# Optimization experiments

Hardware: AMD Instinct MI355X
Metric: run time of the kernel (lower is better)

## Reference

```python
import jax, jax.numpy as jnp
import numpy as np

B, T, D = 8, 4096, 768

def setup_inputs() -> dict:
    key = jax.random.key(0)
    k1, k2, k3, k4, k5, k6 = jax.random.split(key, 6)
    inputs = jax.random.normal(k1, (B, T, D), dtype=jnp.float32)
    mask = jax.random.randint(k2, (B, T), 0, 2, dtype=jnp.int32)
    s = 1.0 / np.sqrt(D)
    Wq_w = jax.random.normal(k3, (D, D), dtype=jnp.float32) * s
    Wq_b = jax.random.normal(k4, (D,), dtype=jnp.float32) * 0.02
    Wk_w = jax.random.normal(k5, (D, D), dtype=jnp.float32) * s
    Wk_b = jax.random.normal(k6, (D,), dtype=jnp.float32) * 0.02
    return {"inputs": inputs, "mask": mask, "Wq_w": Wq_w, "Wq_b": Wq_b, "Wk_w": Wk_w, "Wk_b": Wk_b}

def reference(inputs, mask, Wq_w, Wq_b, Wk_w, Wk_b):
    # Linear layers (torch: x @ W.T + b)
    query = jnp.einsum('btd,ed->bte', inputs, Wq_w) + Wq_b  # (b,t,d)
    key = jnp.einsum('btd,ed->bte', inputs, Wk_w) + Wk_b    # (b,t,d)
    d_k = query.shape[-1]
    scores = jnp.einsum('bqd,bkd->bqk', query, key) / jnp.sqrt(jnp.float32(d_k))  # (b,t,t)
    # mask.unsqueeze(1): (b,1,t) broadcast over query rows
    scores = jnp.where(mask[:, None, :] == 0, jnp.float32(-1e9), scores)
    weights = jax.nn.softmax(scores, axis=2)  # (b,t,t)
    # einsum 'btd,btt->bd' == diagonal of weights, weighted sum of inputs
    w_diag = jnp.einsum('btt->bt', weights)   # (b,t)
    outputs = jnp.einsum('btd,bt->bd', inputs, w_diag)  # (b,d)
    return outputs
```

## Files before the change

kernel.cpp:

```cpp
#include <hip/hip_runtime.h>

#define BB 8
#define TT 4096
#define DD 768
#define MM (BB*TT)

typedef _Float16 f16;
typedef _Float16 f16x8 __attribute__((ext_vector_type(8)));
typedef float f32x4 __attribute__((ext_vector_type(4)));

typedef __attribute__((address_space(1))) void void_g;
typedef __attribute__((address_space(3))) void void_l;

__device__ __forceinline__ void gload16(const void* g, void* l) {
  __builtin_amdgcn_global_load_lds((void_g*)g, (void_l*)l, 16, 0, 0);
}

__global__ void cvt2_f32_f16(const float* __restrict__ a, const float* __restrict__ b,
                             f16* __restrict__ oa, f16* __restrict__ ob, int n) {
  int i = (blockIdx.x * blockDim.x + threadIdx.x) * 8;
  if (i >= 2 * n) return;
  const float* src = (i < n) ? a : b;
  f16* dst = (i < n) ? oa : ob;
  const int j = (i < n) ? i : i - n;
  float4 x = *(const float4*)(src + j);
  float4 y = *(const float4*)(src + j + 4);
  f16x8 o;
  o[0] = (f16)x.x; o[1] = (f16)x.y; o[2] = (f16)x.z; o[3] = (f16)x.w;
  o[4] = (f16)y.x; o[5] = (f16)y.y; o[6] = (f16)y.z; o[7] = (f16)y.w;
  *(f16x8*)(dst + j) = o;
}

__global__ __launch_bounds__(256)
void compact_mask(const int* __restrict__ mask, int* __restrict__ idx,
                  int* __restrict__ nbv) {
  __shared__ int wcnt[4];
  const int b = blockIdx.x;
  const int w = threadIdx.x >> 6, l = threadIdx.x & 63;
  const int* mb = mask + b * TT + w * 1024;
  int mv[16];
  unsigned long long bal[16];
#pragma unroll
  for (int c = 0; c < 16; ++c) {
    mv[c] = mb[c * 64 + l];
    bal[c] = __ballot(mv[c] != 0);
  }
  int tot = 0;
#pragma unroll
  for (int c = 0; c < 16; ++c) tot += __popcll(bal[c]);
  if (l == 0) wcnt[w] = tot;
  __syncthreads();
  int base = 0;
  for (int ww = 0; ww < w; ++ww) base += wcnt[ww];
#pragma unroll
  for (int c = 0; c < 16; ++c) {
    const int pre = __popcll(bal[c] & ((1ull << l) - 1ull));
    if (mv[c]) idx[b * TT + base + pre] = w * 1024 + c * 64 + l;
    base += __popcll(bal[c]);
  }
  if (w == 3 && l == 0) nbv[b] = base;
}

__global__ __launch_bounds__(256)
void gather_cvt(const float* __restrict__ X, const int* __restrict__ idx,
                const int* __restrict__ nbv, f16* __restrict__ Xc) {
  const int rr = blockIdx.x * 8 + (threadIdx.x >> 5);
  const int b = rr >> 12, j = rr & 4095;
  const int l = threadIdx.x & 31;
  if (j >= nbv[b]) return;
  const float* src = X + ((size_t)b * TT + idx[b * TT + j]) * DD + l * 24;
  f16* dst = Xc + ((size_t)b * TT + j) * DD + l * 24;
#pragma unroll
  for (int c = 0; c < 3; ++c) {
    float4 a = *(const float4*)(src + c * 8);
    float4 d4 = *(const float4*)(src + c * 8 + 4);
    f16x8 o;
    o[0] = (f16)a.x;  o[1] = (f16)a.y;  o[2] = (f16)a.z;  o[3] = (f16)a.w;
    o[4] = (f16)d4.x; o[5] = (f16)d4.y; o[6] = (f16)d4.z; o[7] = (f16)d4.w;
    *(f16x8*)(dst + c * 8) = o;
  }
}

__global__ __launch_bounds__(256, 2)
void proj_qkc2(const f16* __restrict__ Xc,
               const f16* __restrict__ Wqh, const f16* __restrict__ Wkh,
               const float* __restrict__ bq, const float* __restrict__ bk,
               const int* __restrict__ nbv,
               f16* __restrict__ Qf, f16* __restrict__ Kc) {
  const int b  = blockIdx.x >> 6;
  const int m0 = (blockIdx.x & 63) * 64;
  const int nb = nbv[b];
  if (m0 >= ((nb + 63) & ~63)) return;

  __shared__ f16 As[4][64 * 32];
  __shared__ f16 Ws[4][256 * 32];
  const int isK = blockIdx.z;
  const f16* Wh = isK ? Wkh : Wqh;
  const float* bias = isK ? bk : bq;
  const int n0 = blockIdx.y * 256;
  const int t = threadIdx.x;
  const int lane = t & 63;
  const int w = t >> 6;
  const int wn = w * 64;
  const int fr = lane & 15, fq = lane >> 4;
  const int xrd = ((fr >> 1) & 3) << 3;

  f32x4 acc[4][4] = {};

  const int r0 = t >> 2;
  const int c8 = ((t & 3) ^ ((t >> 3) & 3)) * 8;
  const f16* w0 = Wh + (size_t)(n0 + r0) * DD + c8;
  const f16* a0 = Xc + (size_t)b * TT * DD + (size_t)(m0 + r0) * DD + c8;

#define PSTAGE(sl, ks_) do { \
    const int k0_ = (ks_) * 32; \
    gload16(a0 + k0_,                      &As[sl][w * 512]); \
    gload16(w0 + k0_,                      &Ws[sl][w * 512]); \
    gload16(w0 + (size_t)64  * DD + k0_,   &Ws[sl][2048 + w * 512]); \
    gload16(w0 + (size_t)128 * DD + k0_,   &Ws[sl][4096 + w * 512]); \
    gload16(w0 + (size_t)192 * DD + k0_,   &Ws[sl][6144 + w * 512]); \
  } while (0)

  PSTAGE(0, 0);
  PSTAGE(1, 1);
  asm volatile("s_waitcnt vmcnt(5)" ::: "memory");
  __builtin_amdgcn_sched_barrier(0);
  __builtin_amdgcn_s_barrier();

  for (int ks = 0; ks < 24; ++ks) {
    const int sl = ks & 3;
    if (ks + 2 < 24) {
      PSTAGE((ks + 2) & 3, ks + 2);
      asm volatile("s_waitcnt vmcnt(10)" ::: "memory");
    } else if (ks + 1 < 24) {
      asm volatile("s_waitcnt vmcnt(5)" ::: "memory");
    } else {
      asm volatile("s_waitcnt vmcnt(0)" ::: "memory");
    }
    __builtin_amdgcn_sched_barrier(0);
    __builtin_amdgcn_s_barrier();
    __builtin_amdgcn_sched_barrier(0);

    f16x8 a[4], bfr[4];
#pragma unroll
    for (int i = 0; i < 4; ++i)
      a[i] = *(const f16x8*)&As[sl][(((i * 16 + fr) * 32) + fq * 8) ^ xrd];
#pragma unroll
    for (int j = 0; j < 4; ++j)
      bfr[j] = *(const f16x8*)&Ws[sl][(((wn + j * 16 + fr) * 32) + fq * 8) ^ xrd];
    __builtin_amdgcn_s_setprio(1);
#pragma unroll
    for (int i = 0; i < 4; ++i)
#pragma unroll
      for (int j = 0; j < 4; ++j)
        acc[i][j] = __builtin_amdgcn_mfma_f32_16x16x32_f16(a[i], bfr[j], acc[i][j], 0, 0, 0);
    __builtin_amdgcn_s_setprio(0);
    __builtin_amdgcn_sched_barrier(0);
    __builtin_amdgcn_s_barrier();
  }
#undef PSTAGE

#pragma unroll
  for (int j = 0; j < 4; ++j) {
    const int col = n0 + wn + j * 16 + fr;
    const float bv = bias[col];
#pragma unroll
    for (int i = 0; i < 4; ++i) {
#pragma unroll
      for (int r = 0; r < 4; ++r) {
        const int rowc = m0 + i * 16 + fq * 4 + r;
        const f16 v = (f16)(acc[i][j][r] + bv);
        if (!isK) {
          const size_t q = (size_t)b * TT * DD +
              ((((size_t)(rowc >> 6) * 24 + (col >> 5)) * 4 + ((rowc >> 4) & 3)) * 512 +
               ((rowc & 15) + (((col >> 3) & 3) << 4)) * 8 + (col & 7));
          Qf[q] = v;
        } else {
          Kc[(size_t)b * TT * DD + (size_t)rowc * DD + col] = v;
        }
      }
    }
  }
}

__global__ __launch_bounds__(256, 3)
void attn17(const f16* __restrict__ Qf, const f16* __restrict__ K,
            const int* __restrict__ nbv, float* __restrict__ pzv,
            float* __restrict__ sdg) {
  const int bid = blockIdx.x;
  const int qs = bid / 48;
  const int rem = bid % 48;
  const int kh = rem >> 3;
  const int bb = rem & 7;
  const int nb = nbv[bb];
  if (qs * 128 >= nb) return;

  __shared__ f16 Ks[2][128 * 64];
  const int t = threadIdx.x, l = t & 63, w = t >> 6;
  const int wq = w >> 1, wk = w & 1;
  const int fr = l & 15, fq = l >> 4;
  const int q0 = qs * 128;
  const float scale = 0.036084391824351613f;
  const int nkt = (nb + 127) >> 7;
  const int q6 = nkt / 6, r6 = nkt % 6;
  const int cnt = q6 + (kh < r6 ? 1 : 0);
  const int lo  = kh * q6 + (kh < r6 ? kh : r6);
  const int P = cnt * 12;

  const f16* Kg = K + (size_t)bb * TT * DD;
  const f16* qf = Qf + (size_t)bb * TT * DD + (size_t)(qs * 2 + wq) * 49152 + (size_t)l * 8;

  const int c8 = ((t & 3) ^ ((t >> 3) & 3)) * 8;
  const f16* klo = Kg + (size_t)(t >> 2) * DD + c8;
  const f16* khi = klo + (size_t)64 * DD;

  const int sx = (fq ^ ((fr >> 1) & 3)) * 8;
  const int bbase = (wk * 64 + fr) * 32 + sx;

  f32x4 acc[4][4] = {};
  f32x4 zacc[4] = {};
  int im0 = 0, im1 = 0, im2 = 0, im3 = 0;
  f16x8 avA[4], avB[4];

#define STAGE(bf, p_) do { \
    const size_t o0 = (size_t)(lo + (p_) / 12) * 128 * DD + (size_t)(((p_) % 12) * 64); \
    gload16(klo + o0,      &Ks[bf][w * 512]); \
    gload16(khi + o0,      &Ks[bf][2048 + w * 512]); \
    gload16(klo + o0 + 32, &Ks[bf][4096 + w * 512]); \
    gload16(khi + o0 + 32, &Ks[bf][6144 + w * 512]); \
  } while (0)

#define QLOAD(dst, dc_) do { \
    const f16* qp_ = qf + (size_t)(dc_) * 2048; \
    _Pragma("unroll") \
    for (int i = 0; i < 4; ++i) (dst)[i] = *(const f16x8*)(qp_ + i * 512); \
  } while (0)

#define MFMA_ALL(av_, bufv, off_) do { \
    f16x8 bv[4]; \
    _Pragma("unroll") \
    for (int j = 0; j < 4; ++j) bv[j] = *(const f16x8*)&Ks[bufv][(off_) + bbase + j * 512]; \
    __builtin_amdgcn_s_setprio(1); \
    _Pragma("unroll") \
    for (int i = 0; i < 4; ++i) \
      _Pragma("unroll") \
      for (int j = 0; j < 4; ++j) \
        acc[i][j] = __builtin_amdgcn_mfma_f32_16x16x32_f16((av_)[i], bv[j], acc[i][j], 0, 0, 0); \
    __builtin_amdgcn_s_setprio(0); \
  } while (0)

#define KT_EPILOGUE(kt_) do { \
    const float mb0 = im0 ? 0.f : -1e30f; \
    const float mb1 = im1 ? 0.f : -1e30f; \
    const float mb2 = im2 ? 0.f : -1e30f; \
    const float mb3 = im3 ? 0.f : -1e30f; \
    const bool isdiag = ((kt_) == qs); \
    _Pragma("unroll") \
    for (int i = 0; i < 4; ++i) { \
      _Pragma("unroll") \
      for (int rg = 0; rg < 4; ++rg) { \
        float v0 = fmaf(acc[i][0][rg], scale, mb0); \
        float v1 = fmaf(acc[i][1][rg], scale, mb1); \
        float v2 = fmaf(acc[i][2][rg], scale, mb2); \
        float v3 = fmaf(acc[i][3][rg], scale, mb3); \
        if (isdiag) { \
          const int rl = wq * 64 + i * 16 + fq * 4 + rg; \
          const int cl = wk * 64 + fr; \
          if (cl      == rl) sdg[(size_t)bb * TT + q0 + rl] = v0; \
          if (cl + 16 == rl) sdg[(size_t)bb * TT + q0 + rl] = v1; \
          if (cl + 32 == rl) sdg[(size_t)bb * TT + q0 + rl] = v2; \
          if (cl + 48 == rl) sdg[(size_t)bb * TT + q0 + rl] = v3; \
        } \
        zacc[i][rg] += __expf(v0) + __expf(v1) + __expf(v2) + __expf(v3); \
      } \
    } \
    _Pragma("unroll") \
    for (int i = 0; i < 4; ++i) \
      _Pragma("unroll") \
      for (int j = 0; j < 4; ++j) acc[i][j] = (f32x4)(0.f); \
  } while (0)

  STAGE(0, 0);
  QLOAD(avA, 0);
  __syncthreads();

  for (int p = 0; p < P; ++p) {
    const int buf = p & 1;
    const int kt = lo + p / 12, c = p % 12;
    if (c == 0) {
      const int cb0 = kt * 128 + wk * 64 + fr;
      im0 = (cb0 < nb); im1 = (cb0 + 16 < nb);
      im2 = (cb0 + 32 < nb); im3 = (cb0 + 48 < nb);
    }

    QLOAD(avB, 2 * c + 1);
    if (p + 1 < P) STAGE(buf ^ 1, p + 1);
    MFMA_ALL(avA, buf, 0);

    if (p + 1 < P) QLOAD(avA, 2 * (((p + 1) % 12)));
    MFMA_ALL(avB, buf, 4096);

    if (c == 11) KT_EPILOGUE(kt);

    __syncthreads();
  }
#undef STAGE
#undef QLOAD
#undef MFMA_ALL
#undef KT_EPILOGUE

  const int slot = kh * 2 + wk;
#pragma unroll
  for (int i = 0; i < 4; ++i) {
#pragma unroll
    for (int rg = 0; rg < 4; ++rg) {
      float z = zacc[i][rg];
#pragma unroll
      for (int off = 1; off < 16; off <<= 1) z += __shfl_xor(z, off);
      if (fr == 0) {
        const int row = wq * 64 + i * 16 + fq * 4 + rg;
        pzv[(size_t)slot * MM + bb * TT + q0 + row] = z;
      }
    }
  }
}

__global__ void merge12c(const float* __restrict__ pz, const float* __restrict__ sdg,
                         const int* __restrict__ nbv,
                         float* __restrict__ wdiagc, float* __restrict__ out) {
  int i = blockIdx.x * 256 + threadIdx.x;
  if (i < BB * DD) out[i] = 0.f;
  if (i >= MM) return;
  const int b = i >> 12, j = i & 4095;
  if (j >= nbv[b]) { wdiagc[i] = 0.f; return; }
  float Z = 0.f;
#pragma unroll
  for (int s = 0; s < 12; ++s) Z += pz[(size_t)s * MM + i];
  wdiagc[i] = __expf(sdg[i]) / Z;
}

__global__ __launch_bounds__(256)
void out_gemv_c(const f16* __restrict__ Xc, const float* __restrict__ wdiagc,
                const int* __restrict__ nbv, float* __restrict__ out) {
  __shared__ float wsm[256];
  const int b = blockIdx.z;
  const int nb = nbv[b];
  const int tbase = blockIdx.x * 256;
  if (tbase >= nb) return;
  const int d = blockIdx.y * 256 + threadIdx.x;
  wsm[threadIdx.x] = (tbase + threadIdx.x < nb) ? wdiagc[b * TT + tbase + threadIdx.x] : 0.f;
  __syncthreads();
  float acc = 0.f;
  const f16* xp = Xc + (size_t)(b * TT + tbase) * DD + d;
  const int lim = (nb - tbase < 256) ? (nb - tbase) : 256;
  for (int i = 0; i < lim; ++i) acc += (float)xp[(size_t)i * DD] * wsm[i];
  atomicAdd(&out[b * DD + d], acc);
}

__global__ __launch_bounds__(256, 3)
void proj_qk(const float* __restrict__ Af,
             const f16* __restrict__ Wqh, const f16* __restrict__ Wkh,
             const float* __restrict__ bq, const float* __restrict__ bk,
             f16* __restrict__ Qf, f16* __restrict__ Kh) {
  __shared__ f16 As[2][64 * 32];
  __shared__ f16 Ws[2][256 * 32];
  const int isK = blockIdx.z;
  const f16* Wh = isK ? Wkh : Wqh;
  const float* bias = isK ? bk : bq;
  const int m0 = blockIdx.x * 64;
  const int n0 = blockIdx.y * 256;
  const int t = threadIdx.x;
  const int lane = t & 63;
  const int w = t >> 6;
  const int wn = w * 64;
  const int fr = lane & 15, fq = lane >> 4;
  const int xst = ((t >> 3) & 3) << 3;
  const int xrd = ((fr >> 1) & 3) << 3;
  f32x4 acc[4][4] = {};
  const int r0 = t >> 2, cA = (t & 3) * 8;
  const int e0 = t * 8;
  const int c8 = ((t & 3) ^ ((t >> 3) & 3)) * 8;
  const f16* w0 = Wh + (size_t)(n0 + r0) * DD + c8;

#define PSTAGE(bf, ks_) do { \
    const int k0_ = (ks_) * 32; \
    gload16(w0 + k0_,                      &Ws[bf][w * 512]); \
    gload16(w0 + (size_t)64  * DD + k0_,   &Ws[bf][2048 + w * 512]); \
    gload16(w0 + (size_t)128 * DD + k0_,   &Ws[bf][4096 + w * 512]); \
    gload16(w0 + (size_t)192 * DD + k0_,   &Ws[bf][6144 + w * 512]); \
    { \
      const float* g0 = Af + (size_t)(m0 + r0) * DD + k0_ + cA; \
      float4 x0 = *(const float4*)g0, x1 = *(const float4*)(g0 + 4); \
      f16x8 va; \
      va[0] = (f16)x0.x; va[1] = (f16)x0.y; va[2] = (f16)x0.z; va[3] = (f16)x0.w; \
      va[4] = (f16)x1.x; va[5] = (f16)x1.y; va[6] = (f16)x1.z; va[7] = (f16)x1.w; \
      *(f16x8*)&As[bf][e0 ^ xst] = va; \
    } \
  } while (0)

  PSTAGE(0, 0);
  __syncthreads();
  for (int ks = 0; ks < 24; ++ks) {
    const int bf = ks & 1;
    if (ks + 1 < 24) PSTAGE(bf ^ 1, ks + 1);
    f16x8 a[4], b[4];
#pragma unroll
    for (int i = 0; i < 4; ++i)
      a[i] = *(const f16x8*)&As[bf][(((i * 16 + fr) * 32) + fq * 8) ^ xrd];
#pragma unroll
    for (int j = 0; j < 4; ++j)
      b[j] = *(const f16x8*)&Ws[bf][(((wn + j * 16 + fr) * 32) + fq * 8) ^ xrd];
#pragma unroll
    for (int i = 0; i < 4; ++i)
#pragma unroll
      for (int j = 0; j < 4; ++j)
        acc[i][j] = __builtin_amdgcn_mfma_f32_16x16x32_f16(a[i], b[j], acc[i][j], 0, 0, 0);
    __syncthreads();
  }
#undef PSTAGE
#pragma unroll
  for (int j = 0; j < 4; ++j) {
    const int col = n0 + wn + j * 16 + fr;
    const float bv = bias[col];
#pragma unroll
    for (int i = 0; i < 4; ++i) {
#pragma unroll
      for (int r = 0; r < 4; ++r) {
        const int row = m0 + i * 16 + fq * 4 + r;
        const f16 v = (f16)(acc[i][j][r] + bv);
        if (!isK) {
          const size_t idxq = (((size_t)(row >> 6) * 24 + (col >> 5)) * 4 +
                              ((row >> 4) & 3)) * 512 +
                             ((row & 15) + (((col >> 3) & 3) << 4)) * 8 + (col & 7);
          Qf[idxq] = v;
        } else {
          Kh[(size_t)row * DD + col] = v;
        }
      }
    }
  }
}

__global__ __launch_bounds__(256, 3)
void attn15(const f16* __restrict__ Qf, const f16* __restrict__ K,
            const int* __restrict__ mask, float* __restrict__ pzv,
            float* __restrict__ sdg) {
  __shared__ f16 Ks[2][128 * 64];
  const int bid = blockIdx.x;
  const int qs = bid / 24;
  const int kh = (bid % 24) >> 3;
  const int bb = bid & 7;
  const int t = threadIdx.x, l = t & 63, w = t >> 6;
  const int wq = w >> 1, wk = w & 1;
  const int fr = l & 15, fq = l >> 4;
  const int q0 = qs * 128;
  const float scale = 0.036084391824351613f;
  const int lo = kh * 11;
  const int cnt = (kh < 2) ? 11 : 10;
  const int P = cnt * 12;
  const f16* Kg = K + (size_t)bb * TT * DD;
  const int grp = bb * 64 + qs * 2 + wq;
  const f16* qf = Qf + (size_t)grp * 24 * 4 * 512 + (size_t)l * 8;
  const int c8 = ((t & 3) ^ ((t >> 3) & 3)) * 8;
  const f16* klo = Kg + (size_t)(t >> 2) * DD + c8;
  const f16* khi = klo + (size_t)64 * DD;
  const int sx = (fq ^ ((fr >> 1) & 3)) * 8;
  const int bbase = (wk * 64 + fr) * 32 + sx;
  f32x4 acc[4][4] = {};
  f32x4 zacc[4] = {};
  int im0 = 1, im1 = 1, im2 = 1, im3 = 1;
  f16x8 avA[4], avB[4];

#define STAGE(bf, p_) do { \
    const size_t o0 = (size_t)(lo + (p_) / 12) * 128 * DD + (size_t)(((p_) % 12) * 64); \
    gload16(klo + o0,      &Ks[bf][w * 512]); \
    gload16(khi + o0,      &Ks[bf][2048 + w * 512]); \
    gload16(klo + o0 + 32, &Ks[bf][4096 + w * 512]); \
    gload16(khi + o0 + 32, &Ks[bf][6144 + w * 512]); \
  } while (0)
#define QLOAD(dst, dc_) do { \
    const f16* qp_ = qf + (size_t)(dc_) * 2048; \
    _Pragma("unroll") \
    for (int i = 0; i < 4; ++i) (dst)[i] = *(const f16x8*)(qp_ + i * 512); \
  } while (0)
#define MFMA_ALL(av_, bufv, off_) do { \
    f16x8 bv[4]; \
    _Pragma("unroll") \
    for (int j = 0; j < 4; ++j) bv[j] = *(const f16x8*)&Ks[bufv][(off_) + bbase + j * 512]; \
    __builtin_amdgcn_s_setprio(1); \
    _Pragma("unroll") \
    for (int i = 0; i < 4; ++i) \
      _Pragma("unroll") \
      for (int j = 0; j < 4; ++j) \
        acc[i][j] = __builtin_amdgcn_mfma_f32_16x16x32_f16((av_)[i], bv[j], acc[i][j], 0, 0, 0); \
    __builtin_amdgcn_s_setprio(0); \
  } while (0)
#define KT_EPILOGUE(kt_) do { \
    const float mb0 = im0 ? 0.f : -1e30f; \
    const float mb1 = im1 ? 0.f : -1e30f; \
    const float mb2 = im2 ? 0.f : -1e30f; \
    const float mb3 = im3 ? 0.f : -1e30f; \
    const bool isdiag = ((kt_) == qs); \
    _Pragma("unroll") \
    for (int i = 0; i < 4; ++i) { \
      _Pragma("unroll") \
      for (int rg = 0; rg < 4; ++rg) { \
        float v0 = fmaf(acc[i][0][rg], scale, mb0); \
        float v1 = fmaf(acc[i][1][rg], scale, mb1); \
        float v2 = fmaf(acc[i][2][rg], scale, mb2); \
        float v3 = fmaf(acc[i][3][rg], scale, mb3); \
        if (isdiag) { \
          const int rl = wq * 64 + i * 16 + fq * 4 + rg; \
          const int cl = wk * 64 + fr; \
          if (cl      == rl) sdg[(size_t)bb * TT + q0 + rl] = v0; \
          if (cl + 16 == rl) sdg[(size_t)bb * TT + q0 + rl] = v1; \
          if (cl + 32 == rl) sdg[(size_t)bb * TT + q0 + rl] = v2; \
          if (cl + 48 == rl) sdg[(size_t)bb * TT + q0 + rl] = v3; \
        } \
        zacc[i][rg] += __expf(v0) + __expf(v1) + __expf(v2) + __expf(v3); \
      } \
    } \
    _Pragma("unroll") \
    for (int i = 0; i < 4; ++i) \
      _Pragma("unroll") \
      for (int j = 0; j < 4; ++j) acc[i][j] = (f32x4)(0.f); \
  } while (0)

  STAGE(0, 0);
  QLOAD(avA, 0);
  __syncthreads();
  for (int p = 0; p < P; ++p) {
    const int buf = p & 1;
    const int kt = lo + p / 12, c = p % 12;
    if (c == 0) {
      const int kb = bb * TT + kt * 128 + wk * 64 + fr;
      im0 = mask[kb]; im1 = mask[kb + 16]; im2 = mask[kb + 32]; im3 = mask[kb + 48];
    }
    QLOAD(avB, 2 * c + 1);
    if (p + 1 < P) STAGE(buf ^ 1, p + 1);
    MFMA_ALL(avA, buf, 0);
    if (p + 1 < P) QLOAD(avA, 2 * (((p + 1) % 12)));
    MFMA_ALL(avB, buf, 4096);
    if (c == 11) KT_EPILOGUE(kt);
    __syncthreads();
  }
#undef STAGE
#undef QLOAD
#undef MFMA_ALL
#undef KT_EPILOGUE
  const int slot = kh * 2 + wk;
#pragma unroll
  for (int i = 0; i < 4; ++i) {
#pragma unroll
    for (int rg = 0; rg < 4; ++rg) {
      float z = zacc[i][rg];
#pragma unroll
      for (int off = 1; off < 16; off <<= 1) z += __shfl_xor(z, off);
      if (fr == 0) {
        const int row = wq * 64 + i * 16 + fq * 4 + rg;
        pzv[(size_t)slot * MM + bb * TT + q0 + row] = z;
      }
    }
  }
}

__global__ void merge6(const float* __restrict__ pz, const float* __restrict__ sdg,
                       float* __restrict__ wdiag, float* __restrict__ out) {
  int i = blockIdx.x * 256 + threadIdx.x;
  if (i < BB * DD) out[i] = 0.f;
  if (i >= MM) return;
  float Z = 0.f;
#pragma unroll
  for (int s = 0; s < 6; ++s) Z += pz[(size_t)s * MM + i];
  wdiag[i] = __expf(sdg[i]) / Z;
}

__global__ __launch_bounds__(256)
void out_gemv(const float* __restrict__ X, const float* __restrict__ wdiag,
              float* __restrict__ out) {
  __shared__ float wsm[256];
  const int b = blockIdx.z;
  const int d = blockIdx.y * 256 + threadIdx.x;
  const int tbase = blockIdx.x * 256;
  wsm[threadIdx.x] = wdiag[b * TT + tbase + threadIdx.x];
  __syncthreads();
  float acc = 0.f;
  const float* xp = X + (size_t)(b * TT + tbase) * DD + d;
#pragma unroll 4
  for (int i = 0; i < 256; ++i) acc += xp[(size_t)i * DD] * wsm[i];
  atomicAdd(&out[b * DD + d], acc);
}

extern "C" void kernel_launch(void* const* d_in, const int* in_sizes, int n_in,
                              void* d_out, int out_size, void* d_ws, size_t ws_size,
                              hipStream_t stream) {
  const float* X    = (const float*)d_in[0];
  const int*   mask = (const int*)d_in[1];
  const float* Wq_w = (const float*)d_in[2];
  const float* Wq_b = (const float*)d_in[3];
  const float* Wk_w = (const float*)d_in[4];
  const float* Wk_b = (const float*)d_in[5];
  float* out = (float*)d_out;

  const size_t n2 = (size_t)MM * DD;
  const size_t wde = (size_t)DD * DD;

  char* p = (char*)d_ws;
  f16* Qf = (f16*)p;            p += n2 * sizeof(f16);
  f16* Kc = (f16*)p;            p += n2 * sizeof(f16);
  f16* Xc = (f16*)p;            p += n2 * sizeof(f16);
  f16* Wqh = (f16*)p;           p += wde * sizeof(f16);
  f16* Wkh = (f16*)p;           p += wde * sizeof(f16);
  int* idx = (int*)p;           p += (size_t)MM * sizeof(int);
  int* nbv = (int*)p;           p += 64;
  float* pz = (float*)p;        p += (size_t)12 * MM * sizeof(float);
  float* sdg = (float*)p;       p += (size_t)MM * sizeof(float);
  float* wdiagc = (float*)p;    p += (size_t)MM * sizeof(float);
  const size_t need_new = (size_t)(p - (char*)d_ws);
  const bool useNew = ws_size >= need_new;

  if (useNew) {
    compact_mask<<<8, 256, 0, stream>>>(mask, idx, nbv);
    cvt2_f32_f16<<<576, 256, 0, stream>>>(Wq_w, Wk_w, Wqh, Wkh, DD * DD);
    gather_cvt<<<4096, 256, 0, stream>>>(X, idx, nbv, Xc);
    proj_qkc2<<<dim3(512, 3, 2), 256, 0, stream>>>(Xc, Wqh, Wkh, Wq_b, Wk_b,
                                                   nbv, Qf, Kc);
    attn17<<<1536, 256, 0, stream>>>(Qf, Kc, nbv, pz, sdg);
    merge12c<<<128, 256, 0, stream>>>(pz, sdg, nbv, wdiagc, out);
    out_gemv_c<<<dim3(16, 3, 8), 256, 0, stream>>>(Xc, wdiagc, nbv, out);
  } else {
    f16* Qf2 = (f16*)d_ws;
    f16* Kh2 = Qf2 + n2;
    f16* Wqh2 = Kh2 + n2;
    f16* Wkh2 = Wqh2 + wde;
    float* pz2 = (float*)Wqh2;
    float* sdg2 = pz2 + 6 * (size_t)MM;
    float* wdiag2 = sdg2 + MM;
    cvt2_f32_f16<<<576, 256, 0, stream>>>(Wq_w, Wk_w, Wqh2, Wkh2, DD * DD);
    proj_qk<<<dim3(512, 3, 2), 256, 0, stream>>>(X, Wqh2, Wkh2, Wq_b, Wk_b,
                                                 Qf2, Kh2);
    attn15<<<768, 256, 0, stream>>>(Qf2, Kh2, mask, pz2, sdg2);
    merge6<<<128, 256, 0, stream>>>(pz2, sdg2, wdiag2, out);
    out_gemv<<<dim3(16, 3, 8), 256, 0, stream>>>(X, wdiag2, out);
  }
}
```

Measured before the change: 258.3 us.

## Fold Wq·Wk into one matrix and use compacted X as keys

Rewrites the scores as X Wq^T Wk X^T plus key-side bias terms. It precomputes M = Wq^T Wk with a small GEMM, projects only Y = X M, and uses the compacted f16 X directly as K. Terms that are constant per query row cancel in the softmax, so only a per-key bias vector (bq·Wk·x) is added in the attention epilogue. This halves the projection GEMM work and removes the K buffer, at the cost of small extra kernels and different f16 rounding of the product matrix. The old fallback path is dropped.

Result: no change. 261.4 us (+1.2%).

```diff
diff --git a/kernel.cpp b/kernel.cpp
--- a/kernel.cpp
+++ b/kernel.cpp
@@ -14,21 +14,6 @@
 
 __device__ __forceinline__ void gload16(const void* g, void* l) {
   __builtin_amdgcn_global_load_lds((void_g*)g, (void_l*)l, 16, 0, 0);
-}
-
-__global__ void cvt2_f32_f16(const float* __restrict__ a, const float* __restrict__ b,
-                             f16* __restrict__ oa, f16* __restrict__ ob, int n) {
-  int i = (blockIdx.x * blockDim.x + threadIdx.x) * 8;
-  if (i >= 2 * n) return;
-  const float* src = (i < n) ? a : b;
-  f16* dst = (i < n) ? oa : ob;
-  const int j = (i < n) ? i : i - n;
-  float4 x = *(const float4*)(src + j);
-  float4 y = *(const float4*)(src + j + 4);
-  f16x8 o;
-  o[0] = (f16)x.x; o[1] = (f16)x.y; o[2] = (f16)x.z; o[3] = (f16)x.w;
-  o[4] = (f16)y.x; o[5] = (f16)y.y; o[6] = (f16)y.z; o[7] = (f16)y.w;
-  *(f16x8*)(dst + j) = o;
 }
 
 __global__ __launch_bounds__(256)
@@ -62,14 +47,44 @@
 }
 
 __global__ __launch_bounds__(256)
-void gather_cvt(const float* __restrict__ X, const int* __restrict__ idx,
-                const int* __restrict__ nbv, f16* __restrict__ Xc) {
+void cvt2T(const float* __restrict__ a, const float* __restrict__ b,
+           f16* __restrict__ oaT, f16* __restrict__ obT) {
+  __shared__ float tile[64][65];
+  const float* src = blockIdx.z ? b : a;
+  f16* dst = blockIdx.z ? obT : oaT;
+  const int n0 = blockIdx.x * 64, d0 = blockIdx.y * 64;
+  const int r = threadIdx.x >> 6, c = threadIdx.x & 63;
+#pragma unroll
+  for (int k = 0; k < 16; ++k)
+    tile[k * 4 + r][c] = src[(size_t)(n0 + k * 4 + r) * DD + d0 + c];
+  __syncthreads();
+#pragma unroll
+  for (int k = 0; k < 16; ++k)
+    dst[(size_t)(d0 + k * 4 + r) * DD + n0 + c] = (f16)tile[c][k * 4 + r];
+}
+
+__global__ __launch_bounds__(256)
+void evec_k(const float* __restrict__ Wk, const float* __restrict__ bq,
+            float* __restrict__ e) {
+  const int d = blockIdx.x * 256 + threadIdx.x;
+  float acc = 0.f;
+  for (int n = 0; n < DD; ++n) acc += bq[n] * Wk[(size_t)n * DD + d];
+  e[d] = acc;
+}
+
+__global__ __launch_bounds__(256)
+void gather_cvt2(const float* __restrict__ X, const int* __restrict__ idx,
+                 const int* __restrict__ nbv, const float* __restrict__ e,
+                 f16* __restrict__ Xc, float* __restrict__ vb) {
   const int rr = blockIdx.x * 8 + (threadIdx.x >> 5);
   const int b = rr >> 12, j = rr & 4095;
   const int l = threadIdx.x & 31;
   if (j >= nbv[b]) return;
+  const float scale = 0.036084391824351613f;
   const float* src = X + ((size_t)b * TT + idx[b * TT + j]) * DD + l * 24;
   f16* dst = Xc + ((size_t)b * TT + j) * DD + l * 24;
+  const float* ep = e + l * 24;
+  float vp = 0.f;
 #pragma unroll
   for (int c = 0; c < 3; ++c) {
     float4 a = *(const float4*)(src + c * 8);
@@ -78,25 +93,22 @@
     o[0] = (f16)a.x;  o[1] = (f16)a.y;  o[2] = (f16)a.z;  o[3] = (f16)a.w;
     o[4] = (f16)d4.x; o[5] = (f16)d4.y; o[6] = (f16)d4.z; o[7] = (f16)d4.w;
     *(f16x8*)(dst + c * 8) = o;
-  }
-}
-
-__global__ __launch_bounds__(256, 2)
-void proj_qkc2(const f16* __restrict__ Xc,
-               const f16* __restrict__ Wqh, const f16* __restrict__ Wkh,
-               const float* __restrict__ bq, const float* __restrict__ bk,
-               const int* __restrict__ nbv,
-               f16* __restrict__ Qf, f16* __restrict__ Kc) {
-  const int b  = blockIdx.x >> 6;
-  const int m0 = (blockIdx.x & 63) * 64;
-  const int nb = nbv[b];
-  if (m0 >= ((nb + 63) & ~63)) return;
-
-  __shared__ f16 As[4][64 * 32];
-  __shared__ f16 Ws[4][256 * 32];
-  const int isK = blockIdx.z;
-  const f16* Wh = isK ? Wkh : Wqh;
-  const float* bias = isK ? bk : bq;
+    vp += a.x * ep[c * 8]     + a.y * ep[c * 8 + 1] +
+          a.z * ep[c * 8 + 2] + a.w * ep[c * 8 + 3] +
+          d4.x * ep[c * 8 + 4] + d4.y * ep[c * 8 + 5] +
+          d4.z * ep[c * 8 + 6] + d4.w * ep[c * 8 + 7];
+  }
+#pragma unroll
+  for (int off = 1; off < 32; off <<= 1) vp += __shfl_xor(vp, off);
+  if (l == 0) vb[b * TT + j] = vp * scale;
+}
+
+__global__ __launch_bounds__(256, 3)
+void gemm_mt(const f16* __restrict__ WkT, const f16* __restrict__ WqT,
+             f16* __restrict__ MT) {
+  __shared__ f16 As[2][64 * 32];
+  __shared__ f16 Ws[2][256 * 32];
+  const int m0 = blockIdx.x * 64;
   const int n0 = blockIdx.y * 256;
   const int t = threadIdx.x;
   const int lane = t & 63;
@@ -109,7 +121,75 @@
 
   const int r0 = t >> 2;
   const int c8 = ((t & 3) ^ ((t >> 3) & 3)) * 8;
-  const f16* w0 = Wh + (size_t)(n0 + r0) * DD + c8;
+  const f16* w0 = WqT + (size_t)(n0 + r0) * DD + c8;
+  const f16* a0 = WkT + (size_t)(m0 + r0) * DD + c8;
+
+#define PSTAGE(bf, ks_) do { \
+    const int k0_ = (ks_) * 32; \
+    gload16(a0 + k0_,                      &As[bf][w * 512]); \
+    gload16(w0 + k0_,                      &Ws[bf][w * 512]); \
+    gload16(w0 + (size_t)64  * DD + k0_,   &Ws[bf][2048 + w * 512]); \
+    gload16(w0 + (size_t)128 * DD + k0_,   &Ws[bf][4096 + w * 512]); \
+    gload16(w0 + (size_t)192 * DD + k0_,   &Ws[bf][6144 + w * 512]); \
+  } while (0)
+
+  PSTAGE(0, 0);
+  __syncthreads();
+  for (int ks = 0; ks < 24; ++ks) {
+    const int bf = ks & 1;
+    if (ks + 1 < 24) PSTAGE(bf ^ 1, ks + 1);
+    f16x8 a[4], bfr[4];
+#pragma unroll
+    for (int i = 0; i < 4; ++i)
+      a[i] = *(const f16x8*)&As[bf][(((i * 16 + fr) * 32) + fq * 8) ^ xrd];
+#pragma unroll
+    for (int j = 0; j < 4; ++j)
+      bfr[j] = *(const f16x8*)&Ws[bf][(((wn + j * 16 + fr) * 32) + fq * 8) ^ xrd];
+#pragma unroll
+    for (int i = 0; i < 4; ++i)
+#pragma unroll
+      for (int j = 0; j < 4; ++j)
+        acc[i][j] = __builtin_amdgcn_mfma_f32_16x16x32_f16(a[i], bfr[j], acc[i][j], 0, 0, 0);
+    __syncthreads();
+  }
+#undef PSTAGE
+
+#pragma unroll
+  for (int j = 0; j < 4; ++j) {
+    const int col = n0 + wn + j * 16 + fr;
+#pragma unroll
+    for (int i = 0; i < 4; ++i)
+#pragma unroll
+      for (int r = 0; r < 4; ++r) {
+        const int row = m0 + i * 16 + fq * 4 + r;
+        MT[(size_t)row * DD + col] = (f16)acc[i][j][r];
+      }
+  }
+}
+
+__global__ __launch_bounds__(256, 2)
+void projY(const f16* __restrict__ Xc, const f16* __restrict__ MT,
+           const int* __restrict__ nbv, f16* __restrict__ Yf) {
+  const int b  = blockIdx.x >> 6;
+  const int m0 = (blockIdx.x & 63) * 64;
+  const int nb = nbv[b];
+  if (m0 >= ((nb + 63) & ~63)) return;
+
+  __shared__ f16 As[4][64 * 32];
+  __shared__ f16 Ws[4][256 * 32];
+  const int n0 = blockIdx.y * 256;
+  const int t = threadIdx.x;
+  const int lane = t & 63;
+  const int w = t >> 6;
+  const int wn = w * 64;
+  const int fr = lane & 15, fq = lane >> 4;
+  const int xrd = ((fr >> 1) & 3) << 3;
+
+  f32x4 acc[4][4] = {};
+
+  const int r0 = t >> 2;
+  const int c8 = ((t & 3) ^ ((t >> 3) & 3)) * 8;
+  const f16* w0 = MT + (size_t)(n0 + r0) * DD + c8;
   const f16* a0 = Xc + (size_t)b * TT * DD + (size_t)(m0 + r0) * DD + c8;
 
 #define PSTAGE(sl, ks_) do { \
@@ -163,30 +243,24 @@
 #pragma unroll
   for (int j = 0; j < 4; ++j) {
     const int col = n0 + wn + j * 16 + fr;
-    const float bv = bias[col];
 #pragma unroll
     for (int i = 0; i < 4; ++i) {
 #pragma unroll
       for (int r = 0; r < 4; ++r) {
         const int rowc = m0 + i * 16 + fq * 4 + r;
-        const f16 v = (f16)(acc[i][j][r] + bv);
-        if (!isK) {
-          const size_t q = (size_t)b * TT * DD +
-              ((((size_t)(rowc >> 6) * 24 + (col >> 5)) * 4 + ((rowc >> 4) & 3)) * 512 +
-               ((rowc & 15) + (((col >> 3) & 3) << 4)) * 8 + (col & 7));
-          Qf[q] = v;
-        } else {
-          Kc[(size_t)b * TT * DD + (size_t)rowc * DD + col] = v;
-        }
+        const size_t q = (size_t)b * TT * DD +
+            ((((size_t)(rowc >> 6) * 24 + (col >> 5)) * 4 + ((rowc >> 4) & 3)) * 512 +
+             ((rowc & 15) + (((col >> 3) & 3) << 4)) * 8 + (col & 7));
+        Yf[q] = (f16)acc[i][j][r];
       }
     }
   }
 }
 
 __global__ __launch_bounds__(256, 3)
-void attn17(const f16* __restrict__ Qf, const f16* __restrict__ K,
-            const int* __restrict__ nbv, float* __restrict__ pzv,
-            float* __restrict__ sdg) {
+void attn17b(const f16* __restrict__ Qf, const f16* __restrict__ K,
+             const float* __restrict__ vbias, const int* __restrict__ nbv,
+             float* __restrict__ pzv, float* __restrict__ sdg) {
   const int bid = blockIdx.x;
   const int qs = bid / 48;
   const int rem = bid % 48;
@@ -209,6 +283,7 @@
 
   const f16* Kg = K + (size_t)bb * TT * DD;
   const f16* qf = Qf + (size_t)bb * TT * DD + (size_t)(qs * 2 + wq) * 49152 + (size_t)l * 8;
+  const float* vbp = vbias + bb * TT;
 
   const int c8 = ((t & 3) ^ ((t >> 3) & 3)) * 8;
   const f16* klo = Kg + (size_t)(t >> 2) * DD + c8;
@@ -220,6 +295,7 @@
   f32x4 acc[4][4] = {};
   f32x4 zacc[4] = {};
   int im0 = 0, im1 = 0, im2 = 0, im3 = 0;
+  float vb0 = 0.f, vb1 = 0.f, vb2 = 0.f, vb3 = 0.f;
   f16x8 avA[4], avB[4];
 
 #define STAGE(bf, p_) do { \
@@ -250,10 +326,10 @@
   } while (0)
 
 #define KT_EPILOGUE(kt_) do { \
-    const float mb0 = im0 ? 0.f : -1e30f; \
-    const float mb1 = im1 ? 0.f : -1e30f; \
-    const float mb2 = im2 ? 0.f : -1e30f; \
-    const float mb3 = im3 ? 0.f : -1e30f; \
+    const float mb0 = im0 ? vb0 : -1e30f; \
+    const float mb1 = im1 ? vb1 : -1e30f; \
+    const float mb2 = im2 ? vb2 : -1e30f; \
+    const float mb3 = im3 ? vb3 : -1e30f; \
     const bool isdiag = ((kt_) == qs); \
     _Pragma("unroll") \
     for (int i = 0; i < 4; ++i) { \
@@ -291,6 +367,8 @@
       const int cb0 = kt * 128 + wk * 64 + fr;
       im0 = (cb0 < nb); im1 = (cb0 + 16 < nb);
       im2 = (cb0 + 32 < nb); im3 = (cb0 + 48 < nb);
+      vb0 = vbp[cb0]; vb1 = vbp[cb0 + 16];
+      vb2 = vbp[cb0 + 32]; vb3 = vbp[cb0 + 48];
     }
 
     QLOAD(avB, 2 * c + 1);
@@ -357,240 +435,6 @@
   atomicAdd(&out[b * DD + d], acc);
 }
 
-__global__ __launch_bounds__(256, 3)
-void proj_qk(const float* __restrict__ Af,
-             const f16* __restrict__ Wqh, const f16* __restrict__ Wkh,
-             const float* __restrict__ bq, const float* __restrict__ bk,
-             f16* __restrict__ Qf, f16* __restrict__ Kh) {
-  __shared__ f16 As[2][64 * 32];
-  __shared__ f16 Ws[2][256 * 32];
-  const int isK = blockIdx.z;
-  const f16* Wh = isK ? Wkh : Wqh;
-  const float* bias = isK ? bk : bq;
-  const int m0 = blockIdx.x * 64;
-  const int n0 = blockIdx.y * 256;
-  const int t = threadIdx.x;
-  const int lane = t & 63;
-  const int w = t >> 6;
-  const int wn = w * 64;
-  const int fr = lane & 15, fq = lane >> 4;
-  const int xst = ((t >> 3) & 3) << 3;
-  const int xrd = ((fr >> 1) & 3) << 3;
-  f32x4 acc[4][4] = {};
-  const int r0 = t >> 2, cA = (t & 3) * 8;
-  const int e0 = t * 8;
-  const int c8 = ((t & 3) ^ ((t >> 3) & 3)) * 8;
-  const f16* w0 = Wh + (size_t)(n0 + r0) * DD + c8;
-
-#define PSTAGE(bf, ks_) do { \
-    const int k0_ = (ks_) * 32; \
-    gload16(w0 + k0_,                      &Ws[bf][w * 512]); \
-    gload16(w0 + (size_t)64  * DD + k0_,   &Ws[bf][2048 + w * 512]); \
-    gload16(w0 + (size_t)128 * DD + k0_,   &Ws[bf][4096 + w * 512]); \
-    gload16(w0 + (size_t)192 * DD + k0_,   &Ws[bf][6144 + w * 512]); \
-    { \
-      const float* g0 = Af + (size_t)(m0 + r0) * DD + k0_ + cA; \
-      float4 x0 = *(const float4*)g0, x1 = *(const float4*)(g0 + 4); \
-      f16x8 va; \
-      va[0] = (f16)x0.x; va[1] = (f16)x0.y; va[2] = (f16)x0.z; va[3] = (f16)x0.w; \
-      va[4] = (f16)x1.x; va[5] = (f16)x1.y; va[6] = (f16)x1.z; va[7] = (f16)x1.w; \
-      *(f16x8*)&As[bf][e0 ^ xst] = va; \
-    } \
-  } while (0)
-
-  PSTAGE(0, 0);
-  __syncthreads();
-  for (int ks = 0; ks < 24; ++ks) {
-    const int bf = ks & 1;
-    if (ks + 1 < 24) PSTAGE(bf ^ 1, ks + 1);
-    f16x8 a[4], b[4];
-#pragma unroll
-    for (int i = 0; i < 4; ++i)
-      a[i] = *(const f16x8*)&As[bf][(((i * 16 + fr) * 32) + fq * 8) ^ xrd];
-#pragma unroll
-    for (int j = 0; j < 4; ++j)
-      b[j] = *(const f16x8*)&Ws[bf][(((wn + j * 16 + fr) * 32) + fq * 8) ^ xrd];
-#pragma unroll
-    for (int i = 0; i < 4; ++i)
-#pragma unroll
-      for (int j = 0; j < 4; ++j)
-        acc[i][j] = __builtin_amdgcn_mfma_f32_16x16x32_f16(a[i], b[j], acc[i][j], 0, 0, 0);
-    __syncthreads();
-  }
-#undef PSTAGE
-#pragma unroll
-  for (int j = 0; j < 4; ++j) {
-    const int col = n0 + wn + j * 16 + fr;
-    const float bv = bias[col];
-#pragma unroll
-    for (int i = 0; i < 4; ++i) {
-#pragma unroll
-      for (int r = 0; r < 4; ++r) {
-        const int row = m0 + i * 16 + fq * 4 + r;
-        const f16 v = (f16)(acc[i][j][r] + bv);
-        if (!isK) {
-          const size_t idxq = (((size_t)(row >> 6) * 24 + (col >> 5)) * 4 +
-                              ((row >> 4) & 3)) * 512 +
-                             ((row & 15) + (((col >> 3) & 3) << 4)) * 8 + (col & 7);
-          Qf[idxq] = v;
-        } else {
-          Kh[(size_t)row * DD + col] = v;
-        }
-      }
-    }
-  }
-}
-
-__global__ __launch_bounds__(256, 3)
-void attn15(const f16* __restrict__ Qf, const f16* __restrict__ K,
-            const int* __restrict__ mask, float* __restrict__ pzv,
-            float* __restrict__ sdg) {
-  __shared__ f16 Ks[2][128 * 64];
-  const int bid = blockIdx.x;
-  const int qs = bid / 24;
-  const int kh = (bid % 24) >> 3;
-  const int bb = bid & 7;
-  const int t = threadIdx.x, l = t & 63, w = t >> 6;
-  const int wq = w >> 1, wk = w & 1;
-  const int fr = l & 15, fq = l >> 4;
-  const int q0 = qs * 128;
-  const float scale = 0.036084391824351613f;
-  const int lo = kh * 11;
-  const int cnt = (kh < 2) ? 11 : 10;
-  const int P = cnt * 12;
-  const f16* Kg = K + (size_t)bb * TT * DD;
-  const int grp = bb * 64 + qs * 2 + wq;
-  const f16* qf = Qf + (size_t)grp * 24 * 4 * 512 + (size_t)l * 8;
-  const int c8 = ((t & 3) ^ ((t >> 3) & 3)) * 8;
-  const f16* klo = Kg + (size_t)(t >> 2) * DD + c8;
-  const f16* khi = klo + (size_t)64 * DD;
-  const int sx = (fq ^ ((fr >> 1) & 3)) * 8;
-  const int bbase = (wk * 64 + fr) * 32 + sx;
-  f32x4 acc[4][4] = {};
-  f32x4 zacc[4] = {};
-  int im0 = 1, im1 = 1, im2 = 1, im3 = 1;
-  f16x8 avA[4], avB[4];
-
-#define STAGE(bf, p_) do { \
-    const size_t o0 = (size_t)(lo + (p_) / 12) * 128 * DD + (size_t)(((p_) % 12) * 64); \
-    gload16(klo + o0,      &Ks[bf][w * 512]); \
-    gload16(khi + o0,      &Ks[bf][2048 + w * 512]); \
-    gload16(klo + o0 + 32, &Ks[bf][4096 + w * 512]); \
-    gload16(khi + o0 + 32, &Ks[bf][6144 + w * 512]); \
-  } while (0)
-#define QLOAD(dst, dc_) do { \
-    const f16* qp_ = qf + (size_t)(dc_) * 2048; \
-    _Pragma("unroll") \
-    for (int i = 0; i < 4; ++i) (dst)[i] = *(const f16x8*)(qp_ + i * 512); \
-  } while (0)
-#define MFMA_ALL(av_, bufv, off_) do { \
-    f16x8 bv[4]; \
-    _Pragma("unroll") \
-    for (int j = 0; j < 4; ++j) bv[j] = *(const f16x8*)&Ks[bufv][(off_) + bbase + j * 512]; \
-    __builtin_amdgcn_s_setprio(1); \
-    _Pragma("unroll") \
-    for (int i = 0; i < 4; ++i) \
-      _Pragma("unroll") \
-      for (int j = 0; j < 4; ++j) \
-        acc[i][j] = __builtin_amdgcn_mfma_f32_16x16x32_f16((av_)[i], bv[j], acc[i][j], 0, 0, 0); \
-    __builtin_amdgcn_s_setprio(0); \
-  } while (0)
-#define KT_EPILOGUE(kt_) do { \
-    const float mb0 = im0 ? 0.f : -1e30f; \
-    const float mb1 = im1 ? 0.f : -1e30f; \
-    const float mb2 = im2 ? 0.f : -1e30f; \
-    const float mb3 = im3 ? 0.f : -1e30f; \
-    const bool isdiag = ((kt_) == qs); \
-    _Pragma("unroll") \
-    for (int i = 0; i < 4; ++i) { \
-      _Pragma("unroll") \
-      for (int rg = 0; rg < 4; ++rg) { \
-        float v0 = fmaf(acc[i][0][rg], scale, mb0); \
-        float v1 = fmaf(acc[i][1][rg], scale, mb1); \
-        float v2 = fmaf(acc[i][2][rg], scale, mb2); \
-        float v3 = fmaf(acc[i][3][rg], scale, mb3); \
-        if (isdiag) { \
-          const int rl = wq * 64 + i * 16 + fq * 4 + rg; \
-          const int cl = wk * 64 + fr; \
-          if (cl      == rl) sdg[(size_t)bb * TT + q0 + rl] = v0; \
-          if (cl + 16 == rl) sdg[(size_t)bb * TT + q0 + rl] = v1; \
-          if (cl + 32 == rl) sdg[(size_t)bb * TT + q0 + rl] = v2; \
-          if (cl + 48 == rl) sdg[(size_t)bb * TT + q0 + rl] = v3; \
-        } \
-        zacc[i][rg] += __expf(v0) + __expf(v1) + __expf(v2) + __expf(v3); \
-      } \
-    } \
-    _Pragma("unroll") \
-    for (int i = 0; i < 4; ++i) \
-      _Pragma("unroll") \
-      for (int j = 0; j < 4; ++j) acc[i][j] = (f32x4)(0.f); \
-  } while (0)
-
-  STAGE(0, 0);
-  QLOAD(avA, 0);
-  __syncthreads();
-  for (int p = 0; p < P; ++p) {
-    const int buf = p & 1;
-    const int kt = lo + p / 12, c = p % 12;
-    if (c == 0) {
-      const int kb = bb * TT + kt * 128 + wk * 64 + fr;
-      im0 = mask[kb]; im1 = mask[kb + 16]; im2 = mask[kb + 32]; im3 = mask[kb + 48];
-    }
-    QLOAD(avB, 2 * c + 1);
-    if (p + 1 < P) STAGE(buf ^ 1, p + 1);
-    MFMA_ALL(avA, buf, 0);
-    if (p + 1 < P) QLOAD(avA, 2 * (((p + 1) % 12)));
-    MFMA_ALL(avB, buf, 4096);
-    if (c == 11) KT_EPILOGUE(kt);
-    __syncthreads();
-  }
-#undef STAGE
-#undef QLOAD
-#undef MFMA_ALL
-#undef KT_EPILOGUE
-  const int slot = kh * 2 + wk;
-#pragma unroll
-  for (int i = 0; i < 4; ++i) {
-#pragma unroll
-    for (int rg = 0; rg < 4; ++rg) {
-      float z = zacc[i][rg];
-#pragma unroll
-      for (int off = 1; off < 16; off <<= 1) z += __shfl_xor(z, off);
-      if (fr == 0) {
-        const int row = wq * 64 + i * 16 + fq * 4 + rg;
-        pzv[(size_t)slot * MM + bb * TT + q0 + row] = z;
-      }
-    }
-  }
-}
-
-__global__ void merge6(const float* __restrict__ pz, const float* __restrict__ sdg,
-                       float* __restrict__ wdiag, float* __restrict__ out) {
-  int i = blockIdx.x * 256 + threadIdx.x;
-  if (i < BB * DD) out[i] = 0.f;
-  if (i >= MM) return;
-  float Z = 0.f;
-#pragma unroll
-  for (int s = 0; s < 6; ++s) Z += pz[(size_t)s * MM + i];
-  wdiag[i] = __expf(sdg[i]) / Z;
-}
-
-__global__ __launch_bounds__(256)
-void out_gemv(const float* __restrict__ X, const float* __restrict__ wdiag,
-              float* __restrict__ out) {
-  __shared__ float wsm[256];
-  const int b = blockIdx.z;
-  const int d = blockIdx.y * 256 + threadIdx.x;
-  const int tbase = blockIdx.x * 256;
-  wsm[threadIdx.x] = wdiag[b * TT + tbase + threadIdx.x];
-  __syncthreads();
-  float acc = 0.f;
-  const float* xp = X + (size_t)(b * TT + tbase) * DD + d;
-#pragma unroll 4
-  for (int i = 0; i < 256; ++i) acc += xp[(size_t)i * DD] * wsm[i];
-  atomicAdd(&out[b * DD + d], acc);
-}
-
 extern "C" void kernel_launch(void* const* d_in, const int* in_sizes, int n_in,
                               void* d_out, int out_size, void* d_ws, size_t ws_size,
                               hipStream_t stream) {
@@ -606,41 +450,26 @@
   const size_t wde = (size_t)DD * DD;
 
   char* p = (char*)d_ws;
-  f16* Qf = (f16*)p;            p += n2 * sizeof(f16);
-  f16* Kc = (f16*)p;            p += n2 * sizeof(f16);
-  f16* Xc = (f16*)p;            p += n2 * sizeof(f16);
-  f16* Wqh = (f16*)p;           p += wde * sizeof(f16);
-  f16* Wkh = (f16*)p;           p += wde * sizeof(f16);
+  f16* Yf  = (f16*)p;           p += n2 * sizeof(f16);
+  f16* Xc  = (f16*)p;           p += n2 * sizeof(f16);
+  f16* WqT = (f16*)p;           p += wde * sizeof(f16);
+  f16* WkT = (f16*)p;           p += wde * sizeof(f16);
+  f16* MT  = (f16*)p;           p += wde * sizeof(f16);
+  float* ev = (float*)p;        p += DD * sizeof(float);
   int* idx = (int*)p;           p += (size_t)MM * sizeof(int);
   int* nbv = (int*)p;           p += 64;
+  float* vb = (float*)p;        p += (size_t)MM * sizeof(float);
   float* pz = (float*)p;        p += (size_t)12 * MM * sizeof(float);
   float* sdg = (float*)p;       p += (size_t)MM * sizeof(float);
   float* wdiagc = (float*)p;    p += (size_t)MM * sizeof(float);
-  const size_t need_new = (size_t)(p - (char*)d_ws);
-  const bool useNew = ws_size >= need_new;
-
-  if (useNew) {
-    compact_mask<<<8, 256, 0, stream>>>(mask, idx, nbv);
-    cvt2_f32_f16<<<576, 256, 0, stream>>>(Wq_w, Wk_w, Wqh, Wkh, DD * DD);
-    gather_cvt<<<4096, 256, 0, stream>>>(X, idx, nbv, Xc);
-    proj_qkc2<<<dim3(512, 3, 2), 256, 0, stream>>>(Xc, Wqh, Wkh, Wq_b, Wk_b,
-                                                   nbv, Qf, Kc);
-    attn17<<<1536, 256, 0, stream>>>(Qf, Kc, nbv, pz, sdg);
-    merge12c<<<128, 256, 0, stream>>>(pz, sdg, nbv, wdiagc, out);
-    out_gemv_c<<<dim3(16, 3, 8), 256, 0, stream>>>(Xc, wdiagc, nbv, out);
-  } else {
-    f16* Qf2 = (f16*)d_ws;
-    f16* Kh2 = Qf2 + n2;
-    f16* Wqh2 = Kh2 + n2;
-    f16* Wkh2 = Wqh2 + wde;
-    float* pz2 = (float*)Wqh2;
-    float* sdg2 = pz2 + 6 * (size_t)MM;
-    float* wdiag2 = sdg2 + MM;
-    cvt2_f32_f16<<<576, 256, 0, stream>>>(Wq_w, Wk_w, Wqh2, Wkh2, DD * DD);
-    proj_qk<<<dim3(512, 3, 2), 256, 0, stream>>>(X, Wqh2, Wkh2, Wq_b, Wk_b,
-                                                 Qf2, Kh2);
-    attn15<<<768, 256, 0, stream>>>(Qf2, Kh2, mask, pz2, sdg2);
-    merge6<<<128, 256, 0, stream>>>(pz2, sdg2, wdiag2, out);
-    out_gemv<<<dim3(16, 3, 8), 256, 0, stream>>>(X, wdiag2, out);
-  }
-}
+
+  compact_mask<<<8, 256, 0, stream>>>(mask, idx, nbv);
+  cvt2T<<<dim3(12, 12, 2), 256, 0, stream>>>(Wq_w, Wk_w, WqT, WkT);
+  evec_k<<<3, 256, 0, stream>>>(Wk_w, Wq_b, ev);
+  gather_cvt2<<<4096, 256, 0, stream>>>(X, idx, nbv, ev, Xc, vb);
+  gemm_mt<<<dim3(12, 3), 256, 0, stream>>>(WkT, WqT, MT);
+  projY<<<dim3(512, 3), 256, 0, stream>>>(Xc, MT, nbv, Yf);
+  attn17b<<<1536, 256, 0, stream>>>(Yf, Xc, vb, nbv, pz, sdg);
+  merge12c<<<128, 256, 0, stream>>>(pz, sdg, nbv, wdiagc, out);
+  out_gemv_c<<<dim3(16, 3, 8), 256, 0, stream>>>(Xc, wdiagc, nbv, out);
+}
```
